# Kernel optimization log

Hardware: AMD Instinct MI355X
Metric: run time of the kernel (lower is better)

Reference implementation:

```python
import jax, jax.numpy as jnp
import numpy as np

N_EMBD = 1024
N_HEAD = 16


def setup_inputs() -> dict:
    key = jax.random.key(0)
    k1, k2, k3 = jax.random.split(key, 3)
    B, T, C = 4, 2048, N_EMBD
    x = jax.random.normal(k1, (B, T, C), dtype=jnp.float32)
    # params (bias=False)
    w_attn = jax.random.normal(k2, (C, 3 * C), dtype=jnp.float32) * (C ** -0.5)
    w_proj = jax.random.normal(k3, (C, C), dtype=jnp.float32) * (C ** -0.5)
    return {"x": x, "w_attn": w_attn, "w_proj": w_proj}


def reference(x, w_attn, w_proj):
    B, T, C = x.shape
    H = N_HEAD
    hs = C // H
    qkv = x @ w_attn  # [B,T,3C]
    q, k, v = jnp.split(qkv, 3, axis=-1)
    # [B,H,T,hs]
    q = q.reshape(B, T, H, hs).transpose(0, 2, 1, 3)
    k = k.reshape(B, T, H, hs).transpose(0, 2, 1, 3)
    v = v.reshape(B, T, H, hs).transpose(0, 2, 1, 3)
    wei = jnp.einsum('bhqd,bhkd->bhqk', q, k) * (hs ** -0.5)
    causal = jnp.tril(jnp.ones((T, T), dtype=bool))
    wei = jnp.where(causal[None, None], wei, -jnp.inf)
    wei = jax.nn.softmax(wei, axis=-1)
    # dropout p=0.0 -> identity
    y = jnp.einsum('bhqk,bhkd->bhqd', wei, v)
    y = y.transpose(0, 2, 1, 3).reshape(B, T, C)
    return y @ w_proj
```

## Files before the change

kernel.cpp:

```cpp
#include <hip/hip_runtime.h>
#include <math.h>
#include <stdint.h>

#define B_BATCH 4
#define T_SEQ   2048
#define C_EMB   1024
#define NH      16
#define HS      64

typedef _Float16 half_t;
typedef __attribute__((ext_vector_type(8))) _Float16 half8;
typedef __attribute__((ext_vector_type(4))) _Float16 half4;
typedef __attribute__((ext_vector_type(2))) __fp16 pk16x2;
typedef __attribute__((ext_vector_type(4))) float f32x4;

static __device__ __forceinline__ f32x4 mfma_k16(half4 a, half4 b, f32x4 c) {
#if __has_builtin(__builtin_amdgcn_mfma_f32_16x16x16f16)
    return __builtin_amdgcn_mfma_f32_16x16x16f16(a, b, c, 0, 0, 0);
#else
    half8 a8 = {a.x, a.y, a.z, a.w, (_Float16)0, (_Float16)0, (_Float16)0, (_Float16)0};
    half8 b8 = {b.x, b.y, b.z, b.w, (_Float16)0, (_Float16)0, (_Float16)0, (_Float16)0};
    return __builtin_amdgcn_mfma_f32_16x16x32_f16(a8, b8, c, 0, 0, 0);
#endif
}

static __device__ __forceinline__ void stage16(const void* g, void* lds_base) {
#if __has_builtin(__builtin_amdgcn_global_load_lds)
    __builtin_amdgcn_global_load_lds(
        (const __attribute__((address_space(1))) void*)g,
        (__attribute__((address_space(3))) void*)lds_base, 16, 0, 0);
#else
    const int lane = threadIdx.x & 63;
    ((uint4*)lds_base)[lane] = *(const uint4*)g;
#endif
}

__global__ __launch_bounds__(256) void f32_to_f16k(const float* __restrict__ src,
                                                   half_t* __restrict__ dst, int n8) {
    const int i = blockIdx.x * 256 + threadIdx.x;
    if (i >= n8) return;
    const float4 a = *(const float4*)(src + (size_t)i * 8);
    const float4 b = *(const float4*)(src + (size_t)i * 8 + 4);
    const pk16x2 h0 = __builtin_amdgcn_cvt_pkrtz(a.x, a.y);
    const pk16x2 h1 = __builtin_amdgcn_cvt_pkrtz(a.z, a.w);
    const pk16x2 h2 = __builtin_amdgcn_cvt_pkrtz(b.x, b.y);
    const pk16x2 h3 = __builtin_amdgcn_cvt_pkrtz(b.z, b.w);
    half8 o = {(_Float16)h0.x, (_Float16)h0.y, (_Float16)h1.x, (_Float16)h1.y,
               (_Float16)h2.x, (_Float16)h2.y, (_Float16)h3.x, (_Float16)h3.y};
    *(half8*)(dst + (size_t)i * 8) = o;
}

__global__ __launch_bounds__(256) void transpose_f32_f16(const float* __restrict__ W,
                                                         half_t* __restrict__ WT,
                                                         int K, int N) {
    __shared__ float t[64][65];
    const int k0 = blockIdx.y * 64, n0 = blockIdx.x * 64;
    const int tid = threadIdx.x;
    const int r = tid >> 4, c4 = (tid & 15) * 4;
#pragma unroll
    for (int p = 0; p < 4; ++p) {
        const float4 g = *(const float4*)(W + (size_t)(k0 + p * 16 + r) * N + n0 + c4);
        t[p * 16 + r][c4 + 0] = g.x;
        t[p * 16 + r][c4 + 1] = g.y;
        t[p * 16 + r][c4 + 2] = g.z;
        t[p * 16 + r][c4 + 3] = g.w;
    }
    __syncthreads();
#pragma unroll
    for (int p = 0; p < 4; ++p) {
        const int n = p * 16 + r;
        half4 s = {(_Float16)t[c4 + 0][n], (_Float16)t[c4 + 1][n],
                   (_Float16)t[c4 + 2][n], (_Float16)t[c4 + 3][n]};
        *(half4*)(WT + (size_t)(n0 + n) * K + k0 + c4) = s;
    }
}

template <bool OUT_F16>
__global__ __launch_bounds__(256) void gemm_bt(const half_t* __restrict__ A,
                                               const half_t* __restrict__ Bt,
                                               void* __restrict__ Cout,
                                               int M, int N, int K) {
    __shared__ __align__(16) half_t SM[2 * 128 * 32];
    half_t* As = SM;
    half_t* Bs = SM + 128 * 32;

    const int tid  = threadIdx.x;
    const int lane = tid & 63;
    const int wid  = tid >> 6;
    const int l16  = lane & 15;
    const int quad = lane >> 4;

    const int m0 = blockIdx.y * 128;
    const int n0 = blockIdx.x * 128;
    const int wm = (wid >> 1) * 64;
    const int wn = (wid & 1) * 64;

    const half_t* gA0 = A  + (size_t)(m0 + wid * 16      + (lane >> 2)) * K + (lane & 3) * 8;
    const half_t* gA1 = A  + (size_t)(m0 + wid * 16 + 64 + (lane >> 2)) * K + (lane & 3) * 8;
    const half_t* gB0 = Bt + (size_t)(n0 + wid * 16      + (lane >> 2)) * K + (lane & 3) * 8;
    const half_t* gB1 = Bt + (size_t)(n0 + wid * 16 + 64 + (lane >> 2)) * K + (lane & 3) * 8;

    half_t* lA0 = As + (size_t)wid * 512;
    half_t* lA1 = As + (size_t)(wid + 4) * 512;
    half_t* lB0 = Bs + (size_t)wid * 512;
    half_t* lB1 = Bs + (size_t)(wid + 4) * 512;

    f32x4 acc[4][4];
#pragma unroll
    for (int i = 0; i < 4; ++i)
#pragma unroll
        for (int j = 0; j < 4; ++j) acc[i][j] = (f32x4){0.f, 0.f, 0.f, 0.f};

    for (int k0 = 0; k0 < K; k0 += 32) {
        __syncthreads();
        stage16(gA0 + k0, lA0);
        stage16(gA1 + k0, lA1);
        stage16(gB0 + k0, lB0);
        stage16(gB1 + k0, lB1);
        __syncthreads();

        half8 fa[4], fb[4];
#pragma unroll
        for (int mt = 0; mt < 4; ++mt)
            fa[mt] = *(const half8*)(As + (wm + mt * 16 + l16) * 32 + quad * 8);
#pragma unroll
        for (int nt = 0; nt < 4; ++nt)
            fb[nt] = *(const half8*)(Bs + (wn + nt * 16 + l16) * 32 + quad * 8);
#pragma unroll
        for (int mt = 0; mt < 4; ++mt)
#pragma unroll
            for (int nt = 0; nt < 4; ++nt)
                acc[mt][nt] = __builtin_amdgcn_mfma_f32_16x16x32_f16(
                    fa[mt], fb[nt], acc[mt][nt], 0, 0, 0);
    }

    if constexpr (OUT_F16) {
        __syncthreads();
        float* cw = (float*)SM + wid * 1024;
        const int rrow = lane >> 2;
        const int cseg = (lane & 3) * 16;
#pragma unroll
        for (int mt = 0; mt < 4; ++mt) {
#pragma unroll
            for (int nt = 0; nt < 4; ++nt)
                *(f32x4*)&cw[(nt * 16 + l16) * 16 + quad * 4] = acc[mt][nt];
            half_t tmp[16];
#pragma unroll
            for (int jj = 0; jj < 16; ++jj)
                tmp[jj] = (half_t)cw[(cseg + jj) * 16 + rrow];
            half_t* dst = (half_t*)Cout + (size_t)(m0 + wm + mt * 16 + rrow) * N
                          + n0 + wn + cseg;
            *(half8*)(dst)     = *(const half8*)(tmp);
            *(half8*)(dst + 8) = *(const half8*)(tmp + 8);
        }
    } else {
#pragma unroll
        for (int mt = 0; mt < 4; ++mt)
#pragma unroll
            for (int nt = 0; nt < 4; ++nt)
#pragma unroll
                for (int r = 0; r < 4; ++r) {
                    const size_t row = m0 + wm + mt * 16 + quad * 4 + r;
                    const size_t col = n0 + wn + nt * 16 + l16;
                    ((float*)Cout)[row * N + col] = acc[mt][nt][r];
                }
    }
}

#define KL_STRIDE 72
#define VT_STRIDE 72
#define SCALE_EXP2 0.18033688f

__global__ __launch_bounds__(256, 4) void attn_mfma(const half_t* __restrict__ qkv,
                                                    half_t* __restrict__ y) {
    __shared__ half_t Kl[64 * KL_STRIDE];
    __shared__ half_t Vt[64 * VT_STRIDE];
    __shared__ float Lstat[64];

    const int tid  = threadIdx.x;
    const int wid  = tid >> 6;
    const int lane = tid & 63;
    const int l16  = lane & 15;
    const int quad = lane >> 4;

    const int L = blockIdx.x;
    const int g = L & 63;
    const int s = L >> 6;
    const int h = g & 15;
    const int b = g >> 4;

    const size_t rs = 3 * C_EMB;
    const half_t* qb = qkv + (size_t)b * T_SEQ * rs + h * HS;
    const half_t* kb = qb + C_EMB;
    const half_t* vb = qb + 2 * C_EMB;

    const int srow = tid >> 2;
    const int scol = (tid & 3) * 16;
    const int rp   = tid & 31;
    const int dblk = tid >> 5;

    const int qrel = wid * 16 + l16;

#pragma unroll 1
    for (int j = 0; j < 2; ++j) {
        const int qh = (j == 0) ? (31 - s) : s;
        const int q0 = qh * 64;

        __syncthreads();
        {
            const half_t* src = qb + (size_t)(q0 + srow) * rs + scol;
            half_t* dst = Kl + srow * KL_STRIDE + scol;
            *(half8*)(dst)     = *(const half8*)(src);
            *(half8*)(dst + 8) = *(const half8*)(src + 8);
        }
        __syncthreads();

        half8 aQ[2];
#pragma unroll
        for (int s2 = 0; s2 < 2; ++s2)
            aQ[s2] = *(const half8*)(Kl + (wid * 16 + l16) * KL_STRIDE + s2 * 32 + quad * 8);

        f32x4 O[4];
#pragma unroll
        for (int dt = 0; dt < 4; ++dt) O[dt] = (f32x4){0.f, 0.f, 0.f, 0.f};
        float lw = 0.f;

        for (int kt = 0; kt <= qh; ++kt) {
            const int k0 = kt * 64;
            const bool diag = (kt == qh);
            __syncthreads();

            {
                const half_t* src = kb + (size_t)(k0 + srow) * rs + scol;
                half_t* dst = Kl + srow * KL_STRIDE + scol;
                *(half8*)(dst)     = *(const half8*)(src);
                *(half8*)(dst + 8) = *(const half8*)(src + 8);
            }
            {
                const uint4 va = *(const uint4*)(vb + (size_t)(k0 + 2 * rp) * rs + dblk * 8);
                const uint4 vc = *(const uint4*)(vb + (size_t)(k0 + 2 * rp + 1) * rs + dblk * 8);
                const uint32_t a[4] = {va.x, va.y, va.z, va.w};
                const uint32_t c[4] = {vc.x, vc.y, vc.z, vc.w};
                unsigned short* vts = (unsigned short*)Vt;
#pragma unroll
                for (int u = 0; u < 4; ++u) {
                    const int d0 = dblk * 8 + 2 * u;
                    const uint32_t w0 = (a[u] & 0xffffu) | (c[u] << 16);
                    const uint32_t w1 = (a[u] >> 16) | (c[u] & 0xffff0000u);
                    *(uint32_t*)(vts + (d0 + 0) * VT_STRIDE + 2 * rp) = w0;
                    *(uint32_t*)(vts + (d0 + 1) * VT_STRIDE + 2 * rp) = w1;
                }
            }
            __syncthreads();

#pragma unroll
            for (int mt = 0; mt < 4; ++mt) {
                const half8 aK0 = *(const half8*)(Kl + (mt * 16 + l16) * KL_STRIDE + quad * 8);
                const half8 aK1 = *(const half8*)(Kl + (mt * 16 + l16) * KL_STRIDE + 32 + quad * 8);
                f32x4 sa = (f32x4){0.f, 0.f, 0.f, 0.f};
                sa = __builtin_amdgcn_mfma_f32_16x16x32_f16(aK0, aQ[0], sa, 0, 0, 0);
                sa = __builtin_amdgcn_mfma_f32_16x16x32_f16(aK1, aQ[1], sa, 0, 0, 0);

                const int kbase = mt * 16 + quad * 4;
                float p[4];
#pragma unroll
                for (int r = 0; r < 4; ++r)
                    p[r] = __builtin_amdgcn_exp2f(sa[r] * SCALE_EXP2);
                if (diag) {
#pragma unroll
                    for (int r = 0; r < 4; ++r)
                        if (kbase + r > qrel) p[r] = 0.f;
                }
                lw += (p[0] + p[1]) + (p[2] + p[3]);

                const half4 pa = {(_Float16)p[0], (_Float16)p[1],
                                  (_Float16)p[2], (_Float16)p[3]};
#pragma unroll
                for (int dt = 0; dt < 4; ++dt) {
                    const half4 bV = *(const half4*)(Vt + (dt * 16 + l16) * VT_STRIDE +
                                                     mt * 16 + quad * 4);
                    O[dt] = mfma_k16(pa, bV, O[dt]);
                }
            }
        }

        lw += __shfl_xor(lw, 16);
        lw += __shfl_xor(lw, 32);
        if (quad == 0) Lstat[wid * 16 + l16] = lw;
        __syncthreads();
#pragma unroll
        for (int r = 0; r < 4; ++r) {
            const int rowl = wid * 16 + quad * 4 + r;
            const float inv = 1.f / Lstat[rowl];
#pragma unroll
            for (int dt = 0; dt < 4; ++dt)
                Vt[rowl * VT_STRIDE + dt * 16 + l16] = (half_t)(O[dt][r] * inv);
        }
        __syncthreads();
        {
            half_t* dst = y + ((size_t)b * T_SEQ + q0 + srow) * C_EMB + h * HS + scol;
            const half_t* src = Vt + srow * VT_STRIDE + scol;
            *(half8*)(dst)     = *(const half8*)(src);
            *(half8*)(dst + 8) = *(const half8*)(src + 8);
        }
    }
}

extern "C" void kernel_launch(void* const* d_in, const int* in_sizes, int n_in,
                              void* d_out, int out_size, void* d_ws, size_t ws_size,
                              hipStream_t stream) {
    const float* x      = (const float*)d_in[0];
    const float* w_attn = (const float*)d_in[1];
    const float* w_proj = (const float*)d_in[2];
    float* out = (float*)d_out;

    half_t* xh   = (half_t*)d_ws;
    half_t* waT  = xh   + (size_t)8192 * 1024;
    half_t* wpT  = waT  + (size_t)3072 * 1024;
    half_t* qkvh = wpT  + (size_t)1024 * 1024;
    half_t* yh   = qkvh + (size_t)8192 * 3072;

    f32_to_f16k<<<4096, 256, 0, stream>>>(x, xh, 8192 * 1024 / 8);
    transpose_f32_f16<<<dim3(48, 16), 256, 0, stream>>>(w_attn, waT, 1024, 3072);
    transpose_f32_f16<<<dim3(16, 16), 256, 0, stream>>>(w_proj, wpT, 1024, 1024);

    gemm_bt<true><<<dim3(24, 64), 256, 0, stream>>>(xh, waT, qkvh, 8192, 3072, 1024);

    attn_mfma<<<dim3(1024), 256, 0, stream>>>(qkvh, yh);

    gemm_bt<false><<<dim3(8, 64), 256, 0, stream>>>(yh, wpT, out, 8192, 1024, 1024);
}
```

Baseline: 276.7 us.

## Merge prep kernels into one launch and use 64-row tiles for output projection

Folds the activation conversion and both weight transposes into a single prep kernel that dispatches by block index, so two kernel launches disappear. Adds a separate output-projection GEMM with 64x128 tiles, which doubles the grid from 512 to 1024 blocks to fill more compute units. The trade-off is less data reuse per block in the projection GEMM, and the merged prep kernel reserves shared memory for every block, including the conversion blocks that never use it.

```diff
diff --git a/kernel.cpp b/kernel.cpp
--- a/kernel.cpp
+++ b/kernel.cpp
@@ -35,27 +35,42 @@
 #endif
 }
 
-__global__ __launch_bounds__(256) void f32_to_f16k(const float* __restrict__ src,
-                                                   half_t* __restrict__ dst, int n8) {
-    const int i = blockIdx.x * 256 + threadIdx.x;
-    if (i >= n8) return;
-    const float4 a = *(const float4*)(src + (size_t)i * 8);
-    const float4 b = *(const float4*)(src + (size_t)i * 8 + 4);
-    const pk16x2 h0 = __builtin_amdgcn_cvt_pkrtz(a.x, a.y);
-    const pk16x2 h1 = __builtin_amdgcn_cvt_pkrtz(a.z, a.w);
-    const pk16x2 h2 = __builtin_amdgcn_cvt_pkrtz(b.x, b.y);
-    const pk16x2 h3 = __builtin_amdgcn_cvt_pkrtz(b.z, b.w);
-    half8 o = {(_Float16)h0.x, (_Float16)h0.y, (_Float16)h1.x, (_Float16)h1.y,
-               (_Float16)h2.x, (_Float16)h2.y, (_Float16)h3.x, (_Float16)h3.y};
-    *(half8*)(dst + (size_t)i * 8) = o;
-}
-
-__global__ __launch_bounds__(256) void transpose_f32_f16(const float* __restrict__ W,
-                                                         half_t* __restrict__ WT,
-                                                         int K, int N) {
+__global__ __launch_bounds__(256) void prep_kernel(const float* __restrict__ x,
+                                                   half_t* __restrict__ xh,
+                                                   const float* __restrict__ wa,
+                                                   half_t* __restrict__ waT,
+                                                   const float* __restrict__ wp,
+                                                   half_t* __restrict__ wpT) {
+    const int blk = blockIdx.x;
+    const int tid = threadIdx.x;
+
+    if (blk < 4096) {
+        const int i = blk * 256 + tid;
+        const float4 a = *(const float4*)(x + (size_t)i * 8);
+        const float4 b = *(const float4*)(x + (size_t)i * 8 + 4);
+        const pk16x2 h0 = __builtin_amdgcn_cvt_pkrtz(a.x, a.y);
+        const pk16x2 h1 = __builtin_amdgcn_cvt_pkrtz(a.z, a.w);
+        const pk16x2 h2 = __builtin_amdgcn_cvt_pkrtz(b.x, b.y);
+        const pk16x2 h3 = __builtin_amdgcn_cvt_pkrtz(b.z, b.w);
+        half8 o = {(_Float16)h0.x, (_Float16)h0.y, (_Float16)h1.x, (_Float16)h1.y,
+                   (_Float16)h2.x, (_Float16)h2.y, (_Float16)h3.x, (_Float16)h3.y};
+        *(half8*)(xh + (size_t)i * 8) = o;
+        return;
+    }
+
+    const float* W;
+    half_t* WT;
+    int K, N, bb;
+    if (blk < 4096 + 768) {
+        bb = blk - 4096; W = wa; WT = waT; K = 1024; N = 3072;
+    } else {
+        bb = blk - 4864; W = wp; WT = wpT; K = 1024; N = 1024;
+    }
+    const int ntiles = N / 64;
+    const int n0 = (bb % ntiles) * 64;
+    const int k0 = (bb / ntiles) * 64;
+
     __shared__ float t[64][65];
-    const int k0 = blockIdx.y * 64, n0 = blockIdx.x * 64;
-    const int tid = threadIdx.x;
     const int r = tid >> 4, c4 = (tid & 15) * 4;
 #pragma unroll
     for (int p = 0; p < 4; ++p) {
@@ -75,11 +90,10 @@
     }
 }
 
-template <bool OUT_F16>
-__global__ __launch_bounds__(256) void gemm_bt(const half_t* __restrict__ A,
-                                               const half_t* __restrict__ Bt,
-                                               void* __restrict__ Cout,
-                                               int M, int N, int K) {
+__global__ __launch_bounds__(256) void gemm_bt_f16(const half_t* __restrict__ A,
+                                                   const half_t* __restrict__ Bt,
+                                                   half_t* __restrict__ Cout,
+                                                   int M, int N, int K) {
     __shared__ __align__(16) half_t SM[2 * 128 * 32];
     half_t* As = SM;
     half_t* Bs = SM + 128 * 32;
@@ -134,37 +148,89 @@
                     fa[mt], fb[nt], acc[mt][nt], 0, 0, 0);
     }
 
-    if constexpr (OUT_F16) {
-        __syncthreads();
-        float* cw = (float*)SM + wid * 1024;
-        const int rrow = lane >> 2;
-        const int cseg = (lane & 3) * 16;
-#pragma unroll
-        for (int mt = 0; mt < 4; ++mt) {
+    __syncthreads();
+    float* cw = (float*)SM + wid * 1024;
+    const int rrow = lane >> 2;
+    const int cseg = (lane & 3) * 16;
+#pragma unroll
+    for (int mt = 0; mt < 4; ++mt) {
+#pragma unroll
+        for (int nt = 0; nt < 4; ++nt)
+            *(f32x4*)&cw[(nt * 16 + l16) * 16 + quad * 4] = acc[mt][nt];
+        half_t tmp[16];
+#pragma unroll
+        for (int jj = 0; jj < 16; ++jj)
+            tmp[jj] = (half_t)cw[(cseg + jj) * 16 + rrow];
+        half_t* dst = Cout + (size_t)(m0 + wm + mt * 16 + rrow) * N + n0 + wn + cseg;
+        *(half8*)(dst)     = *(const half8*)(tmp);
+        *(half8*)(dst + 8) = *(const half8*)(tmp + 8);
+    }
+}
+
+__global__ __launch_bounds__(256) void gemm_bt_a64(const half_t* __restrict__ A,
+                                                   const half_t* __restrict__ Bt,
+                                                   float* __restrict__ Cout,
+                                                   int M, int N, int K) {
+    __shared__ half_t As[64 * 32];
+    __shared__ half_t Bs[128 * 32];
+
+    const int tid  = threadIdx.x;
+    const int lane = tid & 63;
+    const int wid  = tid >> 6;
+    const int l16  = lane & 15;
+    const int quad = lane >> 4;
+
+    const int m0 = blockIdx.y * 64;
+    const int n0 = blockIdx.x * 128;
+    const int wm = (wid & 1) * 32;
+    const int wn = (wid >> 1) * 64;
+
+    const half_t* gA  = A  + (size_t)(m0 + wid * 16      + (lane >> 2)) * K + (lane & 3) * 8;
+    const half_t* gB0 = Bt + (size_t)(n0 + wid * 16      + (lane >> 2)) * K + (lane & 3) * 8;
+    const half_t* gB1 = Bt + (size_t)(n0 + wid * 16 + 64 + (lane >> 2)) * K + (lane & 3) * 8;
+
+    half_t* lA  = As + (size_t)wid * 512;
+    half_t* lB0 = Bs + (size_t)wid * 512;
+    half_t* lB1 = Bs + (size_t)(wid + 4) * 512;
+
+    f32x4 acc[2][4];
+#pragma unroll
+    for (int i = 0; i < 2; ++i)
+#pragma unroll
+        for (int j = 0; j < 4; ++j) acc[i][j] = (f32x4){0.f, 0.f, 0.f, 0.f};
+
+    for (int k0 = 0; k0 < K; k0 += 32) {
+        __syncthreads();
+        stage16(gA + k0, lA);
+        stage16(gB0 + k0, lB0);
+        stage16(gB1 + k0, lB1);
+        __syncthreads();
+
+        half8 fa[2], fb[4];
+#pragma unroll
+        for (int mt = 0; mt < 2; ++mt)
+            fa[mt] = *(const half8*)(As + (wm + mt * 16 + l16) * 32 + quad * 8);
+#pragma unroll
+        for (int nt = 0; nt < 4; ++nt)
+            fb[nt] = *(const half8*)(Bs + (wn + nt * 16 + l16) * 32 + quad * 8);
+#pragma unroll
+        for (int mt = 0; mt < 2; ++mt)
 #pragma unroll
             for (int nt = 0; nt < 4; ++nt)
-                *(f32x4*)&cw[(nt * 16 + l16) * 16 + quad * 4] = acc[mt][nt];
-            half_t tmp[16];
-#pragma unroll
-            for (int jj = 0; jj < 16; ++jj)
-                tmp[jj] = (half_t)cw[(cseg + jj) * 16 + rrow];
-            half_t* dst = (half_t*)Cout + (size_t)(m0 + wm + mt * 16 + rrow) * N
-                          + n0 + wn + cseg;
-            *(half8*)(dst)     = *(const half8*)(tmp);
-            *(half8*)(dst + 8) = *(const half8*)(tmp + 8);
-        }
-    } else {
-#pragma unroll
-        for (int mt = 0; mt < 4; ++mt)
-#pragma unroll
-            for (int nt = 0; nt < 4; ++nt)
-#pragma unroll
-                for (int r = 0; r < 4; ++r) {
-                    const size_t row = m0 + wm + mt * 16 + quad * 4 + r;
-                    const size_t col = n0 + wn + nt * 16 + l16;
-                    ((float*)Cout)[row * N + col] = acc[mt][nt][r];
-                }
-    }
+                acc[mt][nt] = __builtin_amdgcn_mfma_f32_16x16x32_f16(
+                    fa[mt], fb[nt], acc[mt][nt], 0, 0, 0);
+    }
+
+#pragma unroll
+    for (int mt = 0; mt < 2; ++mt)
+#pragma unroll
+        for (int nt = 0; nt < 4; ++nt)
+#pragma unroll
+            for (int r = 0; r < 4; ++r) {
+                const size_t row = m0 + wm + mt * 16 + quad * 4 + r;
+                const size_t col = n0 + wn + nt * 16 + l16;
+                Cout[row * N + col] = acc[mt][nt][r];
+            }
 }
 
 #define KL_STRIDE 72
@@ -320,13 +386,11 @@
     half_t* qkvh = wpT  + (size_t)1024 * 1024;
     half_t* yh   = qkvh + (size_t)8192 * 3072;
 
-    f32_to_f16k<<<4096, 256, 0, stream>>>(x, xh, 8192 * 1024 / 8);
-    transpose_f32_f16<<<dim3(48, 16), 256, 0, stream>>>(w_attn, waT, 1024, 3072);
-    transpose_f32_f16<<<dim3(16, 16), 256, 0, stream>>>(w_proj, wpT, 1024, 1024);
-
-    gemm_bt<true><<<dim3(24, 64), 256, 0, stream>>>(xh, waT, qkvh, 8192, 3072, 1024);
+    prep_kernel<<<5120, 256, 0, stream>>>(x, xh, w_attn, waT, w_proj, wpT);
+
+    gemm_bt_f16<<<dim3(24, 64), 256, 0, stream>>>(xh, waT, qkvh, 8192, 3072, 1024);
 
     attn_mfma<<<dim3(1024), 256, 0, stream>>>(qkvh, yh);
 
-    gemm_bt<false><<<dim3(8, 64), 256, 0, stream>>>(yh, wpT, out, 8192, 1024, 1024);
-}
+    gemm_bt_a64<<<dim3(8, 128), 256, 0, stream>>>(yh, wpT, out, 8192, 1024, 1024);
+}
```

Measured after the change: 276.5 us. About the same (-0.1%).
